# Kernel optimization log

Measured on AMD Instinct MI355X. Metric: run time of the kernel, lower is better.

## Reference

```python
import jax, jax.numpy as jnp
import numpy as np

N_HEADS = 16


def setup_inputs() -> dict:
    key = jax.random.key(0)
    k1, k2, k3 = jax.random.split(key, 3)
    b, t, d = 2, 2048, 1024
    x = jax.random.normal(k1, (b, t, d), dtype=jnp.float32)
    # nn.Linear weights (stored here as [in, out]); 0.02 scale ~ standard init
    w_qkv = jax.random.normal(k2, (d, 3 * d), dtype=jnp.float32) * 0.02
    w_out = jax.random.normal(k3, (d, d), dtype=jnp.float32) * 0.02
    return {"x": x, "w_qkv": w_qkv, "w_out": w_out}


def reference(x, w_qkv, w_out):
    # Causal multi-head self-attention. The original module implements this
    # via a hand-rolled blockwise flash-attention loop with online softmax;
    # the intended math is exactly standard causal SDPA, expressed densely here.
    b, t, d = x.shape
    h = N_HEADS
    hd = d // h
    qkv = (x @ w_qkv).reshape(b, t, 3, h, hd)
    qkv = jnp.transpose(qkv, (2, 0, 3, 1, 4))  # [3, b, h, t, hd]
    q, k, v = qkv[0], qkv[1], qkv[2]
    scale = 1.0 / jnp.sqrt(jnp.float32(hd))
    s = jnp.einsum("bhqd,bhkd->bhqk", q, k) * scale  # [b, h, t, t]
    causal = jnp.tril(jnp.ones((t, t), dtype=bool))
    s = jnp.where(causal, s, -jnp.inf)
    p = jax.nn.softmax(s, axis=-1)
    o = jnp.einsum("bhqk,bhkd->bhqd", p, v)
    o = jnp.transpose(o, (0, 2, 1, 3)).reshape(b, t, d)
    return o @ w_out
```

## Files before the change

### kernel.cpp

```cpp
#include <hip/hip_runtime.h>

typedef float f32x4 __attribute__((ext_vector_type(4)));
typedef short short8 __attribute__((ext_vector_type(8)));
typedef short short4_t __attribute__((ext_vector_type(4)));

#define GLOAD_LDS16(gp, lp) \
  __builtin_amdgcn_global_load_lds((const __attribute__((address_space(1))) void*)(gp), \
                                   (__attribute__((address_space(3))) void*)(lp), 16, 0, 0)

__device__ __forceinline__ short f2bf(float f){
  unsigned u = __builtin_bit_cast(unsigned, f);
  u += 0x7fffu + ((u >> 16) & 1u);
  return (short)(u >> 16);
}

__device__ __forceinline__ float exp2_fast(float x){
  return __builtin_amdgcn_exp2f(x);
}

__global__ void cvt_kernel(const float* __restrict__ x, short* __restrict__ xb, int n4){
  for (int i = blockIdx.x*blockDim.x + threadIdx.x; i < n4; i += gridDim.x*blockDim.x){
    f32x4 v = ((const f32x4*)x)[i];
    short4_t s;
    s[0]=f2bf(v[0]); s[1]=f2bf(v[1]); s[2]=f2bf(v[2]); s[3]=f2bf(v[3]);
    ((short4_t*)xb)[i] = s;
  }
}

__global__ __launch_bounds__(256) void transpose_cvt_kernel(const float* __restrict__ w,
                                                            short* __restrict__ wT,
                                                            int K, int N){
  __shared__ float tile[32][33];
  int bn = blockIdx.x*32, bk = blockIdx.y*32;
  int tx = threadIdx.x & 31, ty = threadIdx.x >> 5;
  #pragma unroll
  for (int r=ty; r<32; r+=8) tile[r][tx] = w[(size_t)(bk+r)*N + bn + tx];
  __syncthreads();
  #pragma unroll
  for (int r=ty; r<32; r+=8) wT[(size_t)(bn+r)*K + bk + tx] = f2bf(tile[tx][r]);
}

template<int MODE>
__global__ __launch_bounds__(256) void gemm128_kernel(
    const short* __restrict__ A, const short* __restrict__ Bt,
    float* __restrict__ Cf, short* __restrict__ qb_, short* __restrict__ kb_,
    short* __restrict__ vtb, int M, int N, int K)
{
  __shared__ short a_lds[128*64];
  __shared__ short b_lds[128*64];
  const int tid = threadIdx.x;
  const int lane = tid & 63;
  const int l15 = lane & 15, lg = lane >> 4;
  const int w  = tid >> 6;
  const int wr = w >> 1, wc = w & 1;
  const int m0 = blockIdx.x * 128, n0 = blockIdx.y * 128;

  f32x4 acc[4][4];
  #pragma unroll
  for (int i=0;i<4;i++)
    #pragma unroll
    for (int j=0;j<4;j++) acc[i][j] = (f32x4){0.f,0.f,0.f,0.f};

  for (int kt = 0; kt < K; kt += 64){
    __syncthreads();
    #pragma unroll
    for (int i=0;i<4;i++){
      int u = i*256 + tid;
      int row = u >> 3, cu = u & 7;
      int kl = ((cu ^ (row & 7)) << 3);
      GLOAD_LDS16(A + (size_t)(m0+row)*K + kt + kl, a_lds + (size_t)(i*256 + (tid & ~63))*8);
    }
    #pragma unroll
    for (int i=0;i<4;i++){
      int u = i*256 + tid;
      int row = u >> 3, cu = u & 7;
      int kl = ((cu ^ (row & 7)) << 3);
      GLOAD_LDS16(Bt + (size_t)(n0+row)*K + kt + kl, b_lds + (size_t)(i*256 + (tid & ~63))*8);
    }
    asm volatile("s_waitcnt vmcnt(0)" ::: "memory");
    __syncthreads();

    #pragma unroll
    for (int kk=0;kk<2;kk++){
      short8 af[4], bfr[4];
      #pragma unroll
      for (int mi=0;mi<4;mi++){
        int row = wr*64 + mi*16 + l15;
        int uu = ((kk*4 + lg) ^ (row & 7));
        af[mi] = *(const short8*)&a_lds[row*64 + uu*8];
      }
      #pragma unroll
      for (int ni=0;ni<4;ni++){
        int row = wc*64 + ni*16 + l15;
        int uu = ((kk*4 + lg) ^ (row & 7));
        bfr[ni] = *(const short8*)&b_lds[row*64 + uu*8];
      }
      #pragma unroll
      for (int mi=0;mi<4;mi++)
        #pragma unroll
        for (int ni=0;ni<4;ni++)
          acc[mi][ni] = __builtin_amdgcn_mfma_f32_16x16x32_bf16(af[mi], bfr[ni], acc[mi][ni], 0,0,0);
    }
  }

  #pragma unroll
  for (int mi=0;mi<4;mi++){
    #pragma unroll
    for (int ni=0;ni<4;ni++){
      int col = n0 + wc*64 + ni*16 + l15;
      #pragma unroll
      for (int r=0;r<4;r++){
        int rowg = m0 + wr*64 + mi*16 + lg*4 + r;
        float v = acc[mi][ni][r];
        if (MODE == 0){
          Cf[(size_t)rowg*N + col] = v;
        } else {
          int three = col >> 10, hh = (col >> 6) & 15, e = col & 63;
          int bb = rowg >> 11, t = rowg & 2047;
          int bh = bb*16 + hh;
          if (three == 0)      qb_[((size_t)bh*2048 + t)*64 + e] = f2bf(v * (0.125f*1.44269504f));
          else if (three == 1) kb_[((size_t)bh*2048 + t)*64 + e] = f2bf(v);
          else                 vtb[((size_t)bh*64 + e)*2048 + t] = f2bf(v);
        }
      }
    }
  }
}

__global__ __launch_bounds__(256) void attn_kernel(
    const short* __restrict__ q, const short* __restrict__ kbuf,
    const short* __restrict__ vt, short* __restrict__ ob)
{
  __shared__ short k_lds[2][64*64];
  __shared__ short v_lds[2][64*64];
  __shared__ short p_lds[4*16*72];

  const int tid = threadIdx.x, lane = tid & 63, w = tid >> 6;
  const int l15 = lane & 15, lg = lane >> 4;
  const int qb = 31 - (blockIdx.x >> 5);
  const int bh = blockIdx.x & 31;
  const int q0 = qb * 64;

  const short* qg = q + ((size_t)bh*2048 + q0 + w*16 + l15)*64;
  short8 qf[2];
  qf[0] = *(const short8*)(qg + lg*8);
  qf[1] = *(const short8*)(qg + 32 + lg*8);

  f32x4 o_acc[4];
  #pragma unroll
  for (int ct=0;ct<4;ct++) o_acc[ct] = (f32x4){0.f,0.f,0.f,0.f};
  float mreg = -1e30f, lreg = 0.f;

  const short* kg = kbuf + (size_t)bh*2048*64;
  const short* vg = vt   + (size_t)bh*64*2048;
  short* pw_lds = p_lds + w*16*72;

  const int wbase = (tid & ~63)*8;

  auto issue = [&](int kv0, int buf){
    #pragma unroll
    for (int i=0;i<2;i++){
      int u = i*256 + tid;
      int row = u >> 3, cu = u & 7;
      int kl = ((cu ^ (row & 7)) << 3);
      GLOAD_LDS16(kg + (size_t)(kv0+row)*64 + kl, &k_lds[buf][i*2048 + wbase]);
    }
    #pragma unroll
    for (int i=0;i<2;i++){
      int u = i*256 + tid;
      int row = u >> 3, cu = u & 7;
      int kl = ((cu ^ (row & 7)) << 3);
      GLOAD_LDS16(vg + (size_t)row*2048 + kv0 + kl, &v_lds[buf][i*2048 + wbase]);
    }
  };

  const int n = qb + 1;
  issue(0, 0);

  for (int s = 0; s < n; s++){
    const int cur = s & 1;
    if (s + 1 < n){
      issue((s+1)*64, cur ^ 1);
      asm volatile("s_waitcnt vmcnt(4)" ::: "memory");
    } else {
      asm volatile("s_waitcnt vmcnt(0)" ::: "memory");
    }
    __builtin_amdgcn_s_barrier();

    const short* kl_ = &k_lds[cur][0];
    const short* vl_ = &v_lds[cur][0];

    f32x4 sacc[4];
    #pragma unroll
    for (int ct=0;ct<4;ct++) sacc[ct] = (f32x4){0.f,0.f,0.f,0.f};
    #pragma unroll
    for (int kk=0;kk<2;kk++){
      #pragma unroll
      for (int ct=0;ct<4;ct++){
        int row = ct*16 + l15;
        int uu = ((kk*4 + lg) ^ (row & 7));
        short8 kf = *(const short8*)&kl_[row*64 + uu*8];
        sacc[ct] = __builtin_amdgcn_mfma_f32_16x16x32_bf16(kf, qf[kk], sacc[ct], 0,0,0);
      }
    }

    if (s == qb){
      int qloc = w*16 + l15;
      #pragma unroll
      for (int ct=0;ct<4;ct++){
        #pragma unroll
        for (int r=0;r<4;r++)
          if (ct*16 + lg*4 + r > qloc) sacc[ct][r] = -1e30f;
      }
    }

    float mx = -1e30f;
    #pragma unroll
    for (int ct=0;ct<4;ct++)
      #pragma unroll
      for (int r=0;r<4;r++) mx = fmaxf(mx, sacc[ct][r]);
    mx = fmaxf(mx, __shfl_xor(mx, 16));
    mx = fmaxf(mx, __shfl_xor(mx, 32));
    float mnew = fmaxf(mreg, mx);
    float alpha = exp2_fast(mreg - mnew);
    mreg = mnew;

    f32x4 p[4];
    float sum = 0.f;
    #pragma unroll
    for (int ct=0;ct<4;ct++)
      #pragma unroll
      for (int r=0;r<4;r++){
        p[ct][r] = exp2_fast(sacc[ct][r] - mnew);
        sum += p[ct][r];
      }
    sum += __shfl_xor(sum, 16);
    sum += __shfl_xor(sum, 32);
    lreg = lreg*alpha + sum;

    float alphaRow[4];
    #pragma unroll
    for (int r=0;r<4;r++) alphaRow[r] = __shfl(alpha, lg*4 + r);
    #pragma unroll
    for (int ct=0;ct<4;ct++)
      #pragma unroll
      for (int r=0;r<4;r++) o_acc[ct][r] *= alphaRow[r];

    #pragma unroll
    for (int ct=0;ct<4;ct++){
      short4_t s4;
      #pragma unroll
      for (int r=0;r<4;r++) s4[r] = f2bf(p[ct][r]);
      *(short4_t*)&pw_lds[l15*72 + ct*16 + lg*4] = s4;
    }
    asm volatile("s_waitcnt lgkmcnt(0)" ::: "memory");

    #pragma unroll
    for (int kh=0;kh<2;kh++){
      short8 pa = *(const short8*)&pw_lds[l15*72 + kh*32 + lg*8];
      #pragma unroll
      for (int ct=0;ct<4;ct++){
        int row = ct*16 + l15;
        int uu = ((kh*4 + lg) ^ (row & 7));
        short8 vf = *(const short8*)&vl_[row*64 + uu*8];
        o_acc[ct] = __builtin_amdgcn_mfma_f32_16x16x32_bf16(pa, vf, o_acc[ct], 0,0,0);
      }
    }

    __builtin_amdgcn_s_barrier();
  }

  int bb = bh >> 4, hh = bh & 15;
  float lfin[4];
  #pragma unroll
  for (int r=0;r<4;r++) lfin[r] = __shfl(lreg, lg*4 + r);
  #pragma unroll
  for (int r=0;r<4;r++){
    float inv = 1.0f / lfin[r];
    int t = q0 + w*16 + lg*4 + r;
    size_t base = ((size_t)(bb*2048 + t))*1024 + (size_t)hh*64;
    #pragma unroll
    for (int ct=0;ct<4;ct++)
      ob[base + ct*16 + l15] = f2bf(o_acc[ct][r] * inv);
  }
}

extern "C" void kernel_launch(void* const* d_in, const int* in_sizes, int n_in,
                              void* d_out, int out_size, void* d_ws, size_t ws_size,
                              hipStream_t stream) {
  const float* x     = (const float*)d_in[0];
  const float* w_qkv = (const float*)d_in[1];
  const float* w_out = (const float*)d_in[2];
  float* out = (float*)d_out;

  char* ws = (char*)d_ws;
  short* xb    = (short*)(ws);
  short* wqkvT = (short*)(ws + (8u  << 20));
  short* woutT = (short*)(ws + (14u << 20));
  short* qbuf  = (short*)(ws + (16u << 20));
  short* kbuf  = (short*)(ws + (24u << 20));
  short* vtbuf = (short*)(ws + (32u << 20));
  short* obuf  = (short*)(ws + (40u << 20));

  cvt_kernel<<<2048, 256, 0, stream>>>(x, xb, (4096*1024)/4);
  transpose_cvt_kernel<<<dim3(96,32), 256, 0, stream>>>(w_qkv, wqkvT, 1024, 3072);
  transpose_cvt_kernel<<<dim3(32,32), 256, 0, stream>>>(w_out, woutT, 1024, 1024);

  gemm128_kernel<1><<<dim3(32,24), 256, 0, stream>>>(xb, wqkvT, nullptr,
                                                     qbuf, kbuf, vtbuf, 4096, 3072, 1024);
  attn_kernel<<<dim3(1024), 256, 0, stream>>>(qbuf, kbuf, vtbuf, obuf);
  gemm128_kernel<0><<<dim3(32,8), 256, 0, stream>>>(obuf, woutT, out,
                                                    nullptr, nullptr, nullptr, 4096, 1024, 1024);
}
```

Before: 119.3 us.

## Enlarge attention q-tile to 128 rows with 8 waves sharing K/V tiles

The attention kernel now runs 512-thread blocks covering 128 query rows, so each K/V tile loaded into LDS serves twice as many queries. This halves the block count and interleaves heavy and light causal blocks in the launch order. It also precomputes the swizzled LDS read offsets, uses a hardware packed bf16 convert for P, and issues one global-to-LDS load per thread per tile. The cost is that the causal diagonal now spans two KV steps, which wastes some masked work, and the larger blocks may lower occupancy and balance with only 512 blocks.

Measured after the change: 118.8 us. Within noise of the previous version (-0.4%).

```diff
diff --git a/kernel.cpp b/kernel.cpp
--- a/kernel.cpp
+++ b/kernel.cpp
@@ -127,19 +127,20 @@
   }
 }
 
-__global__ __launch_bounds__(256) void attn_kernel(
+__global__ __launch_bounds__(512) void attn_kernel(
     const short* __restrict__ q, const short* __restrict__ kbuf,
     const short* __restrict__ vt, short* __restrict__ ob)
 {
   __shared__ short k_lds[2][64*64];
   __shared__ short v_lds[2][64*64];
-  __shared__ short p_lds[4*16*72];
+  __shared__ short p_lds[8*16*72];
 
   const int tid = threadIdx.x, lane = tid & 63, w = tid >> 6;
   const int l15 = lane & 15, lg = lane >> 4;
-  const int qb = 31 - (blockIdx.x >> 5);
+  const int qi = blockIdx.x >> 5;
+  const int qb = (qi < 8) ? (15 - qi) : (qi - 8);
   const int bh = blockIdx.x & 31;
-  const int q0 = qb * 64;
+  const int q0 = qb * 128;
 
   const short* qg = q + ((size_t)bh*2048 + q0 + w*16 + l15)*64;
   short8 qf[2];
@@ -151,44 +152,43 @@
   for (int ct=0;ct<4;ct++) o_acc[ct] = (f32x4){0.f,0.f,0.f,0.f};
   float mreg = -1e30f, lreg = 0.f;
 
-  const short* kg = kbuf + (size_t)bh*2048*64;
-  const short* vg = vt   + (size_t)bh*64*2048;
-  short* pw_lds = p_lds + w*16*72;
-
+  int rdo[2][4];
+  #pragma unroll
+  for (int kk=0;kk<2;kk++)
+    #pragma unroll
+    for (int ct=0;ct<4;ct++){
+      int row = ct*16 + l15;
+      int uu = (kk*4 + lg) ^ (row & 7);
+      rdo[kk][ct] = (row*64 + uu*8)*2;
+    }
+
+  const int grow = tid >> 3, gcu = tid & 7;
+  const int gkl = ((gcu ^ (grow & 7)) << 3);
+  const short* kp = kbuf + (size_t)bh*2048*64 + (size_t)grow*64   + gkl;
+  const short* vp = vt   + (size_t)bh*64*2048 + (size_t)grow*2048 + gkl;
   const int wbase = (tid & ~63)*8;
 
-  auto issue = [&](int kv0, int buf){
-    #pragma unroll
-    for (int i=0;i<2;i++){
-      int u = i*256 + tid;
-      int row = u >> 3, cu = u & 7;
-      int kl = ((cu ^ (row & 7)) << 3);
-      GLOAD_LDS16(kg + (size_t)(kv0+row)*64 + kl, &k_lds[buf][i*2048 + wbase]);
-    }
-    #pragma unroll
-    for (int i=0;i<2;i++){
-      int u = i*256 + tid;
-      int row = u >> 3, cu = u & 7;
-      int kl = ((cu ^ (row & 7)) << 3);
-      GLOAD_LDS16(vg + (size_t)row*2048 + kv0 + kl, &v_lds[buf][i*2048 + wbase]);
-    }
-  };
-
-  const int n = qb + 1;
-  issue(0, 0);
+  char* pw = (char*)(p_lds + w*16*72);
+  const int pwo = (l15*72 + lg*4)*2;
+  const int pro = (l15*72 + lg*8)*2;
+
+  const int n = 2*qb + 2;
+  GLOAD_LDS16(kp, &k_lds[0][wbase]); kp += 4096;
+  GLOAD_LDS16(vp, &v_lds[0][wbase]); vp += 64;
 
   for (int s = 0; s < n; s++){
     const int cur = s & 1;
     if (s + 1 < n){
-      issue((s+1)*64, cur ^ 1);
-      asm volatile("s_waitcnt vmcnt(4)" ::: "memory");
+      GLOAD_LDS16(kp, &k_lds[cur^1][wbase]); kp += 4096;
+      GLOAD_LDS16(vp, &v_lds[cur^1][wbase]); vp += 64;
+      asm volatile("s_waitcnt vmcnt(2)" ::: "memory");
     } else {
       asm volatile("s_waitcnt vmcnt(0)" ::: "memory");
     }
     __builtin_amdgcn_s_barrier();
 
-    const short* kl_ = &k_lds[cur][0];
-    const short* vl_ = &v_lds[cur][0];
+    const char* kl_ = (const char*)&k_lds[cur][0];
+    const char* vl_ = (const char*)&v_lds[cur][0];
 
     f32x4 sacc[4];
     #pragma unroll
@@ -197,28 +197,27 @@
     for (int kk=0;kk<2;kk++){
       #pragma unroll
       for (int ct=0;ct<4;ct++){
-        int row = ct*16 + l15;
-        int uu = ((kk*4 + lg) ^ (row & 7));
-        short8 kf = *(const short8*)&kl_[row*64 + uu*8];
+        short8 kf = *(const short8*)(kl_ + rdo[kk][ct]);
         sacc[ct] = __builtin_amdgcn_mfma_f32_16x16x32_bf16(kf, qf[kk], sacc[ct], 0,0,0);
       }
     }
 
-    if (s == qb){
+    if (s >= 2*qb){
+      int d = s - 2*qb;
       int qloc = w*16 + l15;
       #pragma unroll
       for (int ct=0;ct<4;ct++){
         #pragma unroll
         for (int r=0;r<4;r++)
-          if (ct*16 + lg*4 + r > qloc) sacc[ct][r] = -1e30f;
-      }
-    }
-
-    float mx = -1e30f;
-    #pragma unroll
-    for (int ct=0;ct<4;ct++)
-      #pragma unroll
-      for (int r=0;r<4;r++) mx = fmaxf(mx, sacc[ct][r]);
+          if (d*64 + ct*16 + lg*4 + r > qloc) sacc[ct][r] = -1e30f;
+      }
+    }
+
+    float m01 = fmaxf(fmaxf(sacc[0][0], sacc[0][1]), fmaxf(sacc[0][2], sacc[0][3]));
+    float m23 = fmaxf(fmaxf(sacc[1][0], sacc[1][1]), fmaxf(sacc[1][2], sacc[1][3]));
+    float m45 = fmaxf(fmaxf(sacc[2][0], sacc[2][1]), fmaxf(sacc[2][2], sacc[2][3]));
+    float m67 = fmaxf(fmaxf(sacc[3][0], sacc[3][1]), fmaxf(sacc[3][2], sacc[3][3]));
+    float mx = fmaxf(fmaxf(m01, m23), fmaxf(m45, m67));
     mx = fmaxf(mx, __shfl_xor(mx, 16));
     mx = fmaxf(mx, __shfl_xor(mx, 32));
     float mnew = fmaxf(mreg, mx);
@@ -248,21 +247,19 @@
 
     #pragma unroll
     for (int ct=0;ct<4;ct++){
-      short4_t s4;
-      #pragma unroll
-      for (int r=0;r<4;r++) s4[r] = f2bf(p[ct][r]);
-      *(short4_t*)&pw_lds[l15*72 + ct*16 + lg*4] = s4;
+      uint2 pk;
+      asm("v_cvt_pk_bf16_f32 %0, %1, %2" : "=v"(pk.x) : "v"(p[ct][0]), "v"(p[ct][1]));
+      asm("v_cvt_pk_bf16_f32 %0, %1, %2" : "=v"(pk.y) : "v"(p[ct][2]), "v"(p[ct][3]));
+      *(uint2*)(pw + pwo + ct*32) = pk;
     }
     asm volatile("s_waitcnt lgkmcnt(0)" ::: "memory");
 
     #pragma unroll
     for (int kh=0;kh<2;kh++){
-      short8 pa = *(const short8*)&pw_lds[l15*72 + kh*32 + lg*8];
+      short8 pa = *(const short8*)(pw + pro + kh*64);
       #pragma unroll
       for (int ct=0;ct<4;ct++){
-        int row = ct*16 + l15;
-        int uu = ((kh*4 + lg) ^ (row & 7));
-        short8 vf = *(const short8*)&vl_[row*64 + uu*8];
+        short8 vf = *(const short8*)(vl_ + rdo[kh][ct]);
         o_acc[ct] = __builtin_amdgcn_mfma_f32_16x16x32_bf16(pa, vf, o_acc[ct], 0,0,0);
       }
     }
@@ -308,7 +305,7 @@
 
   gemm128_kernel<1><<<dim3(32,24), 256, 0, stream>>>(xb, wqkvT, nullptr,
                                                      qbuf, kbuf, vtbuf, 4096, 3072, 1024);
-  attn_kernel<<<dim3(1024), 256, 0, stream>>>(qbuf, kbuf, vtbuf, obuf);
+  attn_kernel<<<dim3(512), 512, 0, stream>>>(qbuf, kbuf, vtbuf, obuf);
   gemm128_kernel<0><<<dim3(32,8), 256, 0, stream>>>(obuf, woutT, out,
                                                     nullptr, nullptr, nullptr, 4096, 1024, 1024);
 }
```
